# Kernel optimization log

Hardware: AMD Instinct MI355X
Metric: run time of the kernel (lower is better)

## Reference

```python
import jax, jax.numpy as jnp
import numpy as np

DIM = 1024
HEADS = 16
HEAD_DIM = DIM // HEADS
SCALE = HEAD_DIM ** -0.5


def setup_inputs() -> dict:
    key = jax.random.key(0)
    ks = jax.random.split(key, 6)
    B, N, C = 2, 2048, DIM
    q = jax.random.normal(ks[0], (B, N, C), dtype=jnp.float32)
    k = jax.random.normal(ks[1], (B, N, C), dtype=jnp.float32)
    v = jax.random.normal(ks[2], (B, N, C), dtype=jnp.float32)
    # torch nn.Linear weights: out = x @ W.T (+ b); qkv has no bias (qkv_bias=False)
    W_qkv = jax.random.normal(ks[3], (3 * C, 3 * C), dtype=jnp.float32) * (3 * C) ** -0.5
    W_proj = jax.random.normal(ks[4], (C, C), dtype=jnp.float32) * C ** -0.5
    b_proj = jax.random.normal(ks[5], (C,), dtype=jnp.float32) * 0.02
    return {"q": q, "k": k, "v": v, "W_qkv": W_qkv, "W_proj": W_proj, "b_proj": b_proj}


def reference(q, k, v, W_qkv, W_proj, b_proj):
    B, N, C = q.shape
    # fused QKV projection on concatenated [q,k,v] -> [B,N,3C]
    qkv = jnp.concatenate([q, k, v], axis=-1) @ W_qkv.T
    qkv = qkv.reshape(B, N, 3, HEADS, HEAD_DIM).transpose(2, 0, 3, 1, 4)  # [3,B,H,N,hd]
    qh, kh, vh = qkv[0], qkv[1], qkv[2]
    attn = jnp.einsum('bhqd,bhkd->bhqk', qh, kh) * SCALE
    attn = jax.nn.softmax(attn, axis=-1)  # attn_drop is identity (p=0)
    x = jnp.einsum('bhqk,bhkd->bhqd', attn, vh)  # [B,H,N,hd]
    x = x.transpose(0, 2, 1, 3).reshape(B, N, C)
    x = x @ W_proj.T + b_proj  # proj_drop is identity (p=0)
    return x
```

## Files before the change

kernel.cpp:

```cpp
#include <hip/hip_runtime.h>
#include <hip/hip_bf16.h>
#include <stdint.h>

#define HEADS 16
#define HD 64
#define SEQ 2048
#define BATCH 2
#define CDIM 1024
#define MROWS (BATCH*SEQ)
#define K3C (3*CDIM)
#define QSCALE 0.1803368801111244f

typedef __bf16 bf16x8 __attribute__((ext_vector_type(8)));
typedef float  f32x4  __attribute__((ext_vector_type(4)));

__device__ __forceinline__ unsigned short f2bf(float f) {
    __hip_bfloat16 h = __float2bfloat16(f);
    return __builtin_bit_cast(unsigned short, h);
}
__device__ __forceinline__ unsigned int pack2bf(float a, float b) {
    return (unsigned int)f2bf(a) | ((unsigned int)f2bf(b) << 16);
}
__device__ __forceinline__ bf16x8 frag(uint4 u) { return __builtin_bit_cast(bf16x8, u); }

__device__ __forceinline__ void async16(const unsigned short* g, unsigned short* lds) {
    __builtin_amdgcn_global_load_lds(
        (const __attribute__((address_space(1))) unsigned int*)g,
        (__attribute__((address_space(3))) unsigned int*)lds, 16, 0, 0);
}

__device__ __forceinline__ void dsr(uint4& d, unsigned addr, unsigned imm) {
    asm volatile("ds_read_b128 %0, %1 offset:%c2" : "=v"(d) : "v"(addr), "i"(imm));
}

__global__ void cast_all(const float* __restrict__ q, const float* __restrict__ k,
                         const float* __restrict__ v, const float* __restrict__ Wq,
                         const float* __restrict__ Wp,
                         unsigned short* __restrict__ A, unsigned short* __restrict__ Wqb,
                         unsigned short* __restrict__ Wpb)
{
    const int bid = blockIdx.x;
    const int t = threadIdx.x;
    if (bid < MROWS) {
        const float* srcs[3] = {q, k, v};
        #pragma unroll
        for (int i = 0; i < 3; ++i) {
            float4 f = *(const float4*)(srcs[i] + (size_t)bid*CDIM + t*4);
            ushort4 s;
            s.x = f2bf(f.x); s.y = f2bf(f.y); s.z = f2bf(f.z); s.w = f2bf(f.w);
            *(ushort4*)(A + (size_t)bid*K3C + i*CDIM + t*4) = s;
        }
    } else if (bid < MROWS + 9216) {
        int idx = (bid - MROWS)*256 + t;
        float4 f = ((const float4*)Wq)[idx];
        ushort4 s;
        s.x = f2bf(f.x); s.y = f2bf(f.y); s.z = f2bf(f.z); s.w = f2bf(f.w);
        ((ushort4*)Wqb)[idx] = s;
    } else {
        int idx = (bid - MROWS - 9216)*256 + t;
        float4 f = ((const float4*)Wp)[idx];
        ushort4 s;
        s.x = f2bf(f.x); s.y = f2bf(f.y); s.z = f2bf(f.z); s.w = f2bf(f.w);
        ((ushort4*)Wpb)[idx] = s;
    }
}

template<int EPI>
__global__ __launch_bounds__(256, 2)
void gemm_bt(const unsigned short* __restrict__ A, const unsigned short* __restrict__ B,
             int M, int N, int K,
             unsigned short* __restrict__ qh, unsigned short* __restrict__ kh,
             unsigned short* __restrict__ vt,
             const float* __restrict__ bias, float* __restrict__ out)
{
    __shared__ __attribute__((aligned(16))) unsigned short As[128*32];
    __shared__ __attribute__((aligned(16))) unsigned short Bs[128*32];
    const int tid  = threadIdx.x;
    const int wave = tid >> 6;
    const int lane = tid & 63;
    const int l15  = lane & 15;
    const int quad = lane >> 4;
    const int wm = (wave >> 1) * 64;
    const int wn = (wave & 1) * 64;
    const int m0 = blockIdx.x * 128;
    const int n0 = blockIdx.y * 128;

    f32x4 acc[4][4] = {};

    const int srow = tid >> 2;
    const int sc8  = (tid & 3) * 8;

    for (int k0 = 0; k0 < K; k0 += 32) {
        #pragma unroll
        for (int t = 0; t < 2; ++t) {
            int row = t*64 + srow;
            const unsigned short* ga = A + (size_t)(m0 + row)*K + k0 + sc8;
            const unsigned short* gb = B + (size_t)(n0 + row)*K + k0 + sc8;
            async16(ga, &As[(t*256 + wave*64)*8]);
            async16(gb, &Bs[(t*256 + wave*64)*8]);
        }
        __syncthreads();
        uint4 af[4], bfv[4];
        #pragma unroll
        for (int i = 0; i < 4; ++i) {
            af[i]  = *(const uint4*)&As[(wm + i*16 + l15)*32 + quad*8];
            bfv[i] = *(const uint4*)&Bs[(wn + i*16 + l15)*32 + quad*8];
        }
        #pragma unroll
        for (int mi = 0; mi < 4; ++mi)
            #pragma unroll
            for (int ni = 0; ni < 4; ++ni)
                acc[mi][ni] = __builtin_amdgcn_mfma_f32_16x16x32_bf16(
                    frag(af[mi]), frag(bfv[ni]), acc[mi][ni], 0, 0, 0);
        __syncthreads();
    }

    if constexpr (EPI == 0) {
        #pragma unroll
        for (int mi = 0; mi < 4; ++mi) {
            int row0 = m0 + wm + mi*16 + quad*4;
            int b  = row0 >> 11;
            int nq = row0 & 2047;
            #pragma unroll
            for (int ni = 0; ni < 4; ++ni) {
                int col   = n0 + wn + ni*16 + l15;
                int which = col >> 10;
                int h     = (col >> 6) & 15;
                int d     = col & 63;
                int bh    = b*HEADS + h;
                if (which == 2) {
                    ushort4 pv;
                    pv.x = f2bf(acc[mi][ni][0]);
                    pv.y = f2bf(acc[mi][ni][1]);
                    pv.z = f2bf(acc[mi][ni][2]);
                    pv.w = f2bf(acc[mi][ni][3]);
                    *(ushort4*)&vt[((size_t)bh*HD + d)*SEQ + nq] = pv;
                } else {
                    unsigned short* dst = (which == 0) ? qh : kh;
                    float sc = (which == 0) ? QSCALE : 1.0f;
                    #pragma unroll
                    for (int r = 0; r < 4; ++r)
                        dst[((size_t)bh*SEQ + nq + r)*HD + d] = f2bf(acc[mi][ni][r] * sc);
                }
            }
        }
    } else {
        #pragma unroll
        for (int mi = 0; mi < 4; ++mi) {
            int row0 = m0 + wm + mi*16 + quad*4;
            #pragma unroll
            for (int ni = 0; ni < 4; ++ni) {
                int col  = n0 + wn + ni*16 + l15;
                float bv = bias[col];
                #pragma unroll
                for (int r = 0; r < 4; ++r)
                    out[(size_t)(row0 + r)*N + col] = acc[mi][ni][r] + bv;
            }
        }
    }
}

#define NT48 48

__global__ __launch_bounds__(512, 2)
void gemm256_qkv(const unsigned short* __restrict__ A, const unsigned short* __restrict__ B,
                 unsigned short* __restrict__ qh, unsigned short* __restrict__ kh,
                 unsigned short* __restrict__ vt)
{
    __shared__ __attribute__((aligned(16))) unsigned short As[2*16384];
    __shared__ __attribute__((aligned(16))) unsigned short Bs[2*16384];

    const int tid  = threadIdx.x;
    const int wave = tid >> 6;
    const int lane = tid & 63;
    const int l15  = lane & 15;
    const int quad = lane >> 4;
    const int wr   = wave >> 2;
    const int wc   = wave & 3;

    const int id  = blockIdx.x;
    const int swz = (id & 7)*24 + (id >> 3);
    const int m0  = (swz & 15) * 256;
    const int n0  = (swz >> 4) * 256;

    int lrr[2], kel[2];
    #pragma unroll
    for (int j = 0; j < 2; ++j) {
        int p  = (j*512 + tid) * 16;
        int st = p >> 10;
        int q  = p & 1023;
        int ql = q ^ (((q >> 9) & 1) << 5);
        lrr[j] = (st >> 1)*16 + (ql >> 6);
        kel[j] = (st & 1)*32 + ((ql & 63) >> 1);
    }
    const int ldsc = wave*64*8;

    auto stageA = [&](int t, int g) {
        unsigned short* dst = As + (t & 1)*16384 + g*8192;
        #pragma unroll
        for (int j = 0; j < 2; ++j) {
            int grow = (lrr[j] >> 6)*128 + g*64 + (lrr[j] & 63);
            async16(A + (size_t)(m0 + grow)*K3C + t*64 + kel[j], dst + j*4096 + ldsc);
        }
    };
    auto stageB = [&](int t, int g) {
        unsigned short* dst = Bs + (t & 1)*16384 + g*8192;
        #pragma unroll
        for (int j = 0; j < 2; ++j) {
            int grow = (lrr[j] >> 5)*64 + g*32 + (lrr[j] & 31);
            async16(B + (size_t)(n0 + grow)*K3C + t*64 + kel[j], dst + j*4096 + ldsc);
        }
    };

    const unsigned lanebyte = (unsigned)((l15*64 + quad*16) ^ ((l15 & 8) << 2));
    const unsigned aAddr = (unsigned)(uintptr_t)&As[0] + lanebyte + (unsigned)(wr*8192);
    const unsigned bAddr = (unsigned)(uintptr_t)&Bs[0] + lanebyte + (unsigned)(wc*4096);

    f32x4 acc[8][4] = {};

    stageA(0, 0); stageB(0, 0); stageA(0, 1); stageB(0, 1);
    stageA(1, 0); stageB(1, 0); stageA(1, 1);
    asm volatile("s_waitcnt vmcnt(6)" ::: "memory");
    __builtin_amdgcn_s_barrier();

    for (int tt = 0; tt < NT48; tt += 2) {
        #pragma unroll
        for (int hb = 0; hb < 2; ++hb) {
            const int t = tt + hb;
            uint4 ar[4][2], bl[2][2], bh[2][2];

            #pragma unroll
            for (int mi = 0; mi < 4; ++mi)
                #pragma unroll
                for (int kc = 0; kc < 2; ++kc)
                    dsr(ar[mi][kc], aAddr, hb*32768 + (mi*2 + kc)*1024);
            #pragma unroll
            for (int ni = 0; ni < 2; ++ni)
                #pragma unroll
                for (int kc = 0; kc < 2; ++kc)
                    dsr(bl[ni][kc], bAddr, hb*32768 + (ni*2 + kc)*1024);
            if (t + 1 < NT48) stageB(t + 1, 1);
            __builtin_amdgcn_s_barrier();
            asm volatile("s_waitcnt lgkmcnt(0)" ::: "memory");
            __builtin_amdgcn_sched_barrier(0);
            __builtin_amdgcn_s_setprio(1);
            #pragma unroll
            for (int mi = 0; mi < 4; ++mi)
                #pragma unroll
                for (int ni = 0; ni < 2; ++ni)
                    #pragma unroll
                    for (int kc = 0; kc < 2; ++kc)
                        acc[mi][ni] = __builtin_amdgcn_mfma_f32_16x16x32_bf16(
                            frag(ar[mi][kc]), frag(bl[ni][kc]), acc[mi][ni], 0, 0, 0);
            __builtin_amdgcn_s_setprio(0);
            __builtin_amdgcn_s_barrier();

            #pragma unroll
            for (int ni = 0; ni < 2; ++ni)
                #pragma unroll
                for (int kc = 0; kc < 2; ++kc)
                    dsr(bh[ni][kc], bAddr, hb*32768 + 16384 + (ni*2 + kc)*1024);
            if (t + 2 < NT48) stageA(t + 2, 0);
            __builtin_amdgcn_s_barrier();
            asm volatile("s_waitcnt lgkmcnt(0)" ::: "memory");
            __builtin_amdgcn_sched_barrier(0);
            __builtin_amdgcn_s_setprio(1);
            #pragma unroll
            for (int mi = 0; mi < 4; ++mi)
                #pragma unroll
                for (int ni = 0; ni < 2; ++ni)
                    #pragma unroll
                    for (int kc = 0; kc < 2; ++kc)
                        acc[mi][ni+2] = __builtin_amdgcn_mfma_f32_16x16x32_bf16(
                            frag(ar[mi][kc]), frag(bh[ni][kc]), acc[mi][ni+2], 0, 0, 0);
            __builtin_amdgcn_s_setprio(0);
            __builtin_amdgcn_s_barrier();

            #pragma unroll
            for (int mi = 0; mi < 4; ++mi)
                #pragma unroll
                for (int kc = 0; kc < 2; ++kc)
                    dsr(ar[mi][kc], aAddr, hb*32768 + 16384 + (mi*2 + kc)*1024);
            if (t + 2 < NT48) stageB(t + 2, 0);
            __builtin_amdgcn_s_barrier();
            asm volatile("s_waitcnt lgkmcnt(0)" ::: "memory");
            __builtin_amdgcn_sched_barrier(0);
            __builtin_amdgcn_s_setprio(1);
            #pragma unroll
            for (int mi = 0; mi < 4; ++mi)
                #pragma unroll
                for (int ni = 0; ni < 2; ++ni)
                    #pragma unroll
                    for (int kc = 0; kc < 2; ++kc)
                        acc[mi+4][ni] = __builtin_amdgcn_mfma_f32_16x16x32_bf16(
                            frag(ar[mi][kc]), frag(bl[ni][kc]), acc[mi+4][ni], 0, 0, 0);
            __builtin_amdgcn_s_setprio(0);
            __builtin_amdgcn_s_barrier();

            if (t + 2 < NT48) stageA(t + 2, 1);
            if (t + 2 < NT48)      { asm volatile("s_waitcnt vmcnt(6)" ::: "memory"); }
            else if (t + 1 < NT48) { asm volatile("s_waitcnt vmcnt(0)" ::: "memory"); }
            __builtin_amdgcn_s_barrier();
            __builtin_amdgcn_s_setprio(1);
            #pragma unroll
            for (int mi = 0; mi < 4; ++mi)
                #pragma unroll
                for (int ni = 0; ni < 2; ++ni)
                    #pragma unroll
                    for (int kc = 0; kc < 2; ++kc)
                        acc[mi+4][ni+2] = __builtin_amdgcn_mfma_f32_16x16x32_bf16(
                            frag(ar[mi][kc]), frag(bh[ni][kc]), acc[mi+4][ni+2], 0, 0, 0);
            __builtin_amdgcn_s_setprio(0);
            __builtin_amdgcn_s_barrier();
        }
    }

    #pragma unroll
    for (int mi = 0; mi < 8; ++mi) {
        const int row0 = m0 + wr*128 + mi*16 + quad*4;
        const int b  = row0 >> 11;
        const int nq = row0 & 2047;
        #pragma unroll
        for (int ni = 0; ni < 4; ++ni) {
            const int col   = n0 + wc*64 + ni*16 + l15;
            const int which = col >> 10;
            const int h     = (col >> 6) & 15;
            const int d     = col & 63;
            const int bh_   = b*HEADS + h;
            if (which == 2) {
                ushort4 pv;
                pv.x = f2bf(acc[mi][ni][0]);
                pv.y = f2bf(acc[mi][ni][1]);
                pv.z = f2bf(acc[mi][ni][2]);
                pv.w = f2bf(acc[mi][ni][3]);
                *(ushort4*)&vt[((size_t)bh_*HD + d)*SEQ + nq] = pv;
            } else {
                unsigned short* dst = (which == 0) ? qh : kh;
                float sc = (which == 0) ? QSCALE : 1.0f;
                #pragma unroll
                for (int r = 0; r < 4; ++r)
                    dst[((size_t)bh_*SEQ + nq + r)*HD + d] = f2bf(acc[mi][ni][r] * sc);
            }
        }
    }
}

__global__ __launch_bounds__(256, 2)
void attention(const unsigned short* __restrict__ qh, const unsigned short* __restrict__ kh,
               const unsigned short* __restrict__ vt, unsigned short* __restrict__ xb)
{
    const int qt = blockIdx.x;
    const int h  = blockIdx.y;
    const int b  = blockIdx.z;
    const int bh = b*HEADS + h;
    const int tid  = threadIdx.x;
    const int wave = tid >> 6;
    const int lane = tid & 63;
    const int l15  = lane & 15;
    const int quad = lane >> 4;

    __shared__ __attribute__((aligned(16))) unsigned short Ks[2][64*64];
    __shared__ __attribute__((aligned(16))) unsigned short Vs[2][64*64];
    __shared__ __attribute__((aligned(16))) unsigned short Ps[4][2*16*72];

    const unsigned short* Qp = qh + ((size_t)bh*SEQ + qt*128 + wave*32)*HD;
    const unsigned short* Kp = kh + (size_t)bh*SEQ*HD;
    const unsigned short* Vp = vt + (size_t)bh*HD*SEQ;

    auto stage = [&](int kt, int bufI) {
        #pragma unroll
        for (int t = 0; t < 2; ++t) {
            int c  = t*256 + wave*64 + lane;
            int r  = c >> 3;
            int cc = (c & 7) ^ (r & 7);
            async16(Kp + (size_t)(kt*64 + r)*HD + cc*8,
                    &Ks[bufI][(t*256 + wave*64)*8]);
            async16(Vp + (size_t)r*SEQ + kt*64 + cc*8,
                    &Vs[bufI][(t*256 + wave*64)*8]);
        }
    };

    stage(0, 0);

    uint4 qf[2][2];
    #pragma unroll
    for (int g = 0; g < 2; ++g) {
        qf[g][0] = *(const uint4*)(Qp + (size_t)(g*16 + l15)*HD + quad*8);
        qf[g][1] = *(const uint4*)(Qp + (size_t)(g*16 + l15)*HD + 32 + quad*8);
    }

    f32x4 o[2][4] = {};
    float m_s[2] = {-INFINITY, -INFINITY};
    float l_s[2] = {0.f, 0.f};

    unsigned short* Pw = Ps[wave];
    const int x7 = l15 & 7;

    for (int kt = 0; kt < SEQ/64; ++kt) {
        stage((kt + 1) & 31, (kt + 1) & 1);
        asm volatile("s_waitcnt vmcnt(4)" ::: "memory");
        asm volatile("s_barrier" ::: "memory");

        const unsigned short* Kb = Ks[kt & 1];
        const unsigned short* Vb = Vs[kt & 1];

        f32x4 s[2][4];
        #pragma unroll
        for (int st = 0; st < 4; ++st) {
            int rb = st*16 + l15;
            uint4 kf0 = *(const uint4*)&Kb[(rb*8 + (quad ^ x7))*8];
            uint4 kf1 = *(const uint4*)&Kb[(rb*8 + ((4 + quad) ^ x7))*8];
            #pragma unroll
            for (int g = 0; g < 2; ++g) {
                f32x4 z = {};
                z = __builtin_amdgcn_mfma_f32_16x16x32_bf16(frag(kf0), frag(qf[g][0]), z, 0, 0, 0);
                z = __builtin_amdgcn_mfma_f32_16x16x32_bf16(frag(kf1), frag(qf[g][1]), z, 0, 0, 0);
                s[g][st] = z;
            }
        }

        #pragma unroll
        for (int g = 0; g < 2; ++g) {
            float mloc = s[g][0][0];
            #pragma unroll
            for (int st = 0; st < 4; ++st)
                #pragma unroll
                for (int r = 0; r < 4; ++r)
                    mloc = fmaxf(mloc, s[g][st][r]);
            mloc = fmaxf(mloc, __shfl_xor(mloc, 16));
            mloc = fmaxf(mloc, __shfl_xor(mloc, 32));

            float mn = fmaxf(m_s[g], mloc);
            float al = __builtin_amdgcn_exp2f(m_s[g] - mn);
            m_s[g] = mn;

            float rs = 0.f;
            float p[4][4];
            #pragma unroll
            for (int st = 0; st < 4; ++st)
                #pragma unroll
                for (int r = 0; r < 4; ++r) {
                    p[st][r] = __builtin_amdgcn_exp2f(s[g][st][r] - mn);
                    rs += p[st][r];
                }
            rs += __shfl_xor(rs, 16);
            rs += __shfl_xor(rs, 32);
            l_s[g] = al*l_s[g] + rs;

            #pragma unroll
            for (int st = 0; st < 4; ++st)
                #pragma unroll
                for (int r = 0; r < 4; ++r)
                    o[g][st][r] *= al;

            #pragma unroll
            for (int st = 0; st < 4; ++st) {
                uint2 pk;
                pk.x = pack2bf(p[st][0], p[st][1]);
                pk.y = pack2bf(p[st][2], p[st][3]);
                *(uint2*)&Pw[g*1152 + l15*72 + st*16 + quad*4] = pk;
            }
        }
        asm volatile("s_waitcnt lgkmcnt(0)" ::: "memory");

        uint4 pB[2][2];
        #pragma unroll
        for (int g = 0; g < 2; ++g) {
            pB[g][0] = *(const uint4*)&Pw[g*1152 + l15*72 + quad*8];
            pB[g][1] = *(const uint4*)&Pw[g*1152 + l15*72 + 32 + quad*8];
        }

        #pragma unroll
        for (int st = 0; st < 4; ++st) {
            int rb = st*16 + l15;
            uint4 vf0 = *(const uint4*)&Vb[(rb*8 + (quad ^ x7))*8];
            uint4 vf1 = *(const uint4*)&Vb[(rb*8 + ((4 + quad) ^ x7))*8];
            #pragma unroll
            for (int g = 0; g < 2; ++g) {
                o[g][st] = __builtin_amdgcn_mfma_f32_16x16x32_bf16(frag(vf0), frag(pB[g][0]), o[g][st], 0, 0, 0);
                o[g][st] = __builtin_amdgcn_mfma_f32_16x16x32_bf16(frag(vf1), frag(pB[g][1]), o[g][st], 0, 0, 0);
            }
        }

        asm volatile("s_barrier" ::: "memory");
    }

    #pragma unroll
    for (int g = 0; g < 2; ++g) {
        float inv = 1.0f / l_s[g];
        #pragma unroll
        for (int st = 0; st < 4; ++st) {
            uint2 pk;
            pk.x = pack2bf(o[g][st][0]*inv, o[g][st][1]*inv);
            pk.y = pack2bf(o[g][st][2]*inv, o[g][st][3]*inv);
            *(uint2*)&Pw[g*1152 + l15*72 + st*16 + quad*4] = pk;
        }
    }
    asm volatile("s_waitcnt lgkmcnt(0)" ::: "memory");

    const int qr = lane >> 2;
    const int dd = (lane & 3) * 16;
    #pragma unroll
    for (int g = 0; g < 2; ++g) {
        uint4 oa = *(const uint4*)&Pw[g*1152 + qr*72 + dd];
        uint4 ob = *(const uint4*)&Pw[g*1152 + qr*72 + dd + 8];
        const int mrow = b*SEQ + qt*128 + wave*32 + g*16 + qr;
        *(uint4*)&xb[(size_t)mrow*CDIM + h*HD + dd]     = oa;
        *(uint4*)&xb[(size_t)mrow*CDIM + h*HD + dd + 8] = ob;
    }
}

extern "C" void kernel_launch(void* const* d_in, const int* in_sizes, int n_in,
                              void* d_out, int out_size, void* d_ws, size_t ws_size,
                              hipStream_t stream)
{
    const float* q  = (const float*)d_in[0];
    const float* k  = (const float*)d_in[1];
    const float* v  = (const float*)d_in[2];
    const float* Wq = (const float*)d_in[3];
    const float* Wp = (const float*)d_in[4];
    const float* bp = (const float*)d_in[5];
    float* out = (float*)d_out;

    char* p = (char*)d_ws;
    auto carve = [&](size_t bytes) { char* r = p; p += (bytes + 255) & ~(size_t)255; return r; };
    unsigned short* Abuf   = (unsigned short*)carve((size_t)MROWS*K3C*2);
    unsigned short* Wqkvb  = (unsigned short*)carve((size_t)K3C*K3C*2);
    unsigned short* Wprojb = (unsigned short*)carve((size_t)CDIM*CDIM*2);
    unsigned short* qhb    = (unsigned short*)carve((size_t)BATCH*HEADS*SEQ*HD*2);
    unsigned short* khb    = (unsigned short*)carve((size_t)BATCH*HEADS*SEQ*HD*2);
    unsigned short* vtb    = (unsigned short*)carve((size_t)BATCH*HEADS*SEQ*HD*2);
    unsigned short* xbuf   = (unsigned short*)carve((size_t)MROWS*CDIM*2);

    cast_all<<<MROWS + 9216 + 1024, 256, 0, stream>>>(q, k, v, Wq, Wp, Abuf, Wqkvb, Wprojb);

    gemm256_qkv<<<dim3(192), 512, 0, stream>>>(Abuf, Wqkvb, qhb, khb, vtb);

    attention<<<dim3(SEQ/128, HEADS, BATCH), 256, 0, stream>>>(qhb, khb, vtb, xbuf);

    gemm_bt<1><<<dim3(MROWS/128, CDIM/128), 256, 0, stream>>>(
        xbuf, Wprojb, MROWS, CDIM, CDIM, nullptr, nullptr, nullptr, bp, out);
}
```

Before: 300.5 us.

## Retile QKV GEMM to 256x192 tiles for 256 blocks matching CU count

The QKV projection GEMM moves from 256x256 tiles (192 blocks) to 256x192 tiles (256 blocks), so the grid matches the 256 CUs of MI355X and fewer CUs sit idle. Staging is simplified to a single per-k-step stage function issuing 7 async loads, placed before the last MFMA phase instead of spread across phases. MFMA loops are reordered so kc is outermost. The smaller N tile lowers arithmetic intensity and reduces how much global-load latency each block can hide.

```diff
diff --git a/kernel.cpp b/kernel.cpp
--- a/kernel.cpp
+++ b/kernel.cpp
@@ -168,7 +168,7 @@
                  unsigned short* __restrict__ vt)
 {
     __shared__ __attribute__((aligned(16))) unsigned short As[2*16384];
-    __shared__ __attribute__((aligned(16))) unsigned short Bs[2*16384];
+    __shared__ __attribute__((aligned(16))) unsigned short Bs[2*12288];
 
     const int tid  = threadIdx.x;
     const int wave = tid >> 6;
@@ -179,137 +179,129 @@
     const int wc   = wave & 3;
 
     const int id  = blockIdx.x;
-    const int swz = (id & 7)*24 + (id >> 3);
+    const int swz = (id & 7)*32 + (id >> 3);
     const int m0  = (swz & 15) * 256;
-    const int n0  = (swz >> 4) * 256;
-
-    int lrr[2], kel[2];
+    const int n0  = (swz >> 4) * 192;
+
+    size_t aSrc[4]; size_t bSrc[3];
     #pragma unroll
-    for (int j = 0; j < 2; ++j) {
-        int p  = (j*512 + tid) * 16;
-        int st = p >> 10;
-        int q  = p & 1023;
+    for (int u = 0; u < 4; ++u) {
+        int P  = u*8192 + tid*16;
+        int st = P >> 10, q = P & 1023;
         int ql = q ^ (((q >> 9) & 1) << 5);
-        lrr[j] = (st >> 1)*16 + (ql >> 6);
-        kel[j] = (st & 1)*32 + ((ql & 63) >> 1);
-    }
-    const int ldsc = wave*64*8;
-
-    auto stageA = [&](int t, int g) {
-        unsigned short* dst = As + (t & 1)*16384 + g*8192;
-        #pragma unroll
-        for (int j = 0; j < 2; ++j) {
-            int grow = (lrr[j] >> 6)*128 + g*64 + (lrr[j] & 63);
-            async16(A + (size_t)(m0 + grow)*K3C + t*64 + kel[j], dst + j*4096 + ldsc);
-        }
+        int row = m0 + (st >> 1)*16 + (ql >> 6);
+        int kel = (st & 1)*32 + ((ql & 63) >> 1);
+        aSrc[u] = (size_t)row*K3C + kel;
+    }
+    #pragma unroll
+    for (int u = 0; u < 3; ++u) {
+        int P  = u*8192 + tid*16;
+        int st = P >> 10, q = P & 1023;
+        int ql = q ^ (((q >> 9) & 1) << 5);
+        int row = n0 + (st >> 1)*16 + (ql >> 6);
+        int kel = (st & 1)*32 + ((ql & 63) >> 1);
+        bSrc[u] = (size_t)row*K3C + kel;
+    }
+    const int wdst = wave*512;
+
+    auto stage = [&](int t) {
+        const int hb = t & 1;
+        #pragma unroll
+        for (int u = 0; u < 4; ++u)
+            async16(A + aSrc[u] + t*64, As + hb*16384 + u*4096 + wdst);
+        #pragma unroll
+        for (int u = 0; u < 3; ++u)
+            async16(B + bSrc[u] + t*64, Bs + hb*12288 + u*4096 + wdst);
     };
-    auto stageB = [&](int t, int g) {
-        unsigned short* dst = Bs + (t & 1)*16384 + g*8192;
-        #pragma unroll
-        for (int j = 0; j < 2; ++j) {
-            int grow = (lrr[j] >> 5)*64 + g*32 + (lrr[j] & 31);
-            async16(B + (size_t)(n0 + grow)*K3C + t*64 + kel[j], dst + j*4096 + ldsc);
-        }
-    };
 
     const unsigned lanebyte = (unsigned)((l15*64 + quad*16) ^ ((l15 & 8) << 2));
-    const unsigned aAddr = (unsigned)(uintptr_t)&As[0] + lanebyte + (unsigned)(wr*8192);
-    const unsigned bAddr = (unsigned)(uintptr_t)&Bs[0] + lanebyte + (unsigned)(wc*4096);
-
-    f32x4 acc[8][4] = {};
-
-    stageA(0, 0); stageB(0, 0); stageA(0, 1); stageB(0, 1);
-    stageA(1, 0); stageB(1, 0); stageA(1, 1);
-    asm volatile("s_waitcnt vmcnt(6)" ::: "memory");
+    const unsigned aAddr = (unsigned)(uintptr_t)&As[0] + lanebyte + (unsigned)(wr*16384);
+    const unsigned bAddr = (unsigned)(uintptr_t)&Bs[0] + lanebyte + (unsigned)(wc*6144);
+
+    f32x4 acc[8][3] = {};
+
+    stage(0); stage(1);
+    asm volatile("s_waitcnt vmcnt(7)" ::: "memory");
     __builtin_amdgcn_s_barrier();
 
     for (int tt = 0; tt < NT48; tt += 2) {
         #pragma unroll
         for (int hb = 0; hb < 2; ++hb) {
             const int t = tt + hb;
-            uint4 ar[4][2], bl[2][2], bh[2][2];
+            uint4 ar[4][2], bl[2][2], bh[2];
 
             #pragma unroll
             for (int mi = 0; mi < 4; ++mi)
                 #pragma unroll
                 for (int kc = 0; kc < 2; ++kc)
-                    dsr(ar[mi][kc], aAddr, hb*32768 + (mi*2 + kc)*1024);
+                    dsr(ar[mi][kc], aAddr, hb*32768 + mi*2048 + kc*1024);
             #pragma unroll
             for (int ni = 0; ni < 2; ++ni)
                 #pragma unroll
                 for (int kc = 0; kc < 2; ++kc)
-                    dsr(bl[ni][kc], bAddr, hb*32768 + (ni*2 + kc)*1024);
-            if (t + 1 < NT48) stageB(t + 1, 1);
+                    dsr(bl[ni][kc], bAddr, hb*24576 + ni*2048 + kc*1024);
             __builtin_amdgcn_s_barrier();
             asm volatile("s_waitcnt lgkmcnt(0)" ::: "memory");
             __builtin_amdgcn_sched_barrier(0);
             __builtin_amdgcn_s_setprio(1);
             #pragma unroll
-            for (int mi = 0; mi < 4; ++mi)
-                #pragma unroll
-                for (int ni = 0; ni < 2; ++ni)
+            for (int kc = 0; kc < 2; ++kc)
+                #pragma unroll
+                for (int mi = 0; mi < 4; ++mi)
                     #pragma unroll
-                    for (int kc = 0; kc < 2; ++kc)
+                    for (int ni = 0; ni < 2; ++ni)
                         acc[mi][ni] = __builtin_amdgcn_mfma_f32_16x16x32_bf16(
                             frag(ar[mi][kc]), frag(bl[ni][kc]), acc[mi][ni], 0, 0, 0);
             __builtin_amdgcn_s_setprio(0);
             __builtin_amdgcn_s_barrier();
 
             #pragma unroll
-            for (int ni = 0; ni < 2; ++ni)
-                #pragma unroll
-                for (int kc = 0; kc < 2; ++kc)
-                    dsr(bh[ni][kc], bAddr, hb*32768 + 16384 + (ni*2 + kc)*1024);
-            if (t + 2 < NT48) stageA(t + 2, 0);
+            for (int kc = 0; kc < 2; ++kc)
+                dsr(bh[kc], bAddr, hb*24576 + 2*2048 + kc*1024);
             __builtin_amdgcn_s_barrier();
             asm volatile("s_waitcnt lgkmcnt(0)" ::: "memory");
             __builtin_amdgcn_sched_barrier(0);
             __builtin_amdgcn_s_setprio(1);
             #pragma unroll
+            for (int kc = 0; kc < 2; ++kc)
+                #pragma unroll
+                for (int mi = 0; mi < 4; ++mi)
+                    acc[mi][2] = __builtin_amdgcn_mfma_f32_16x16x32_bf16(
+                        frag(ar[mi][kc]), frag(bh[kc]), acc[mi][2], 0, 0, 0);
+            __builtin_amdgcn_s_setprio(0);
+            __builtin_amdgcn_s_barrier();
+
+            #pragma unroll
             for (int mi = 0; mi < 4; ++mi)
                 #pragma unroll
-                for (int ni = 0; ni < 2; ++ni)
-                    #pragma unroll
-                    for (int kc = 0; kc < 2; ++kc)
-                        acc[mi][ni+2] = __builtin_amdgcn_mfma_f32_16x16x32_bf16(
-                            frag(ar[mi][kc]), frag(bh[ni][kc]), acc[mi][ni+2], 0, 0, 0);
-            __builtin_amdgcn_s_setprio(0);
-            __builtin_amdgcn_s_barrier();
-
-            #pragma unroll
-            for (int mi = 0; mi < 4; ++mi)
-                #pragma unroll
                 for (int kc = 0; kc < 2; ++kc)
-                    dsr(ar[mi][kc], aAddr, hb*32768 + 16384 + (mi*2 + kc)*1024);
-            if (t + 2 < NT48) stageB(t + 2, 0);
+                    dsr(ar[mi][kc], aAddr, hb*32768 + (4 + mi)*2048 + kc*1024);
             __builtin_amdgcn_s_barrier();
             asm volatile("s_waitcnt lgkmcnt(0)" ::: "memory");
             __builtin_amdgcn_sched_barrier(0);
             __builtin_amdgcn_s_setprio(1);
             #pragma unroll
-            for (int mi = 0; mi < 4; ++mi)
-                #pragma unroll
-                for (int ni = 0; ni < 2; ++ni)
+            for (int kc = 0; kc < 2; ++kc)
+                #pragma unroll
+                for (int mi = 0; mi < 4; ++mi)
                     #pragma unroll
-                    for (int kc = 0; kc < 2; ++kc)
+                    for (int ni = 0; ni < 2; ++ni)
                         acc[mi+4][ni] = __builtin_amdgcn_mfma_f32_16x16x32_bf16(
                             frag(ar[mi][kc]), frag(bl[ni][kc]), acc[mi+4][ni], 0, 0, 0);
             __builtin_amdgcn_s_setprio(0);
             __builtin_amdgcn_s_barrier();
 
-            if (t + 2 < NT48) stageA(t + 2, 1);
-            if (t + 2 < NT48)      { asm volatile("s_waitcnt vmcnt(6)" ::: "memory"); }
+            if (t + 2 < NT48)      { stage(t + 2);
+                                     asm volatile("s_waitcnt vmcnt(7)" ::: "memory"); }
             else if (t + 1 < NT48) { asm volatile("s_waitcnt vmcnt(0)" ::: "memory"); }
             __builtin_amdgcn_s_barrier();
             __builtin_amdgcn_s_setprio(1);
             #pragma unroll
-            for (int mi = 0; mi < 4; ++mi)
-                #pragma unroll
-                for (int ni = 0; ni < 2; ++ni)
-                    #pragma unroll
-                    for (int kc = 0; kc < 2; ++kc)
-                        acc[mi+4][ni+2] = __builtin_amdgcn_mfma_f32_16x16x32_bf16(
-                            frag(ar[mi][kc]), frag(bh[ni][kc]), acc[mi+4][ni+2], 0, 0, 0);
+            for (int kc = 0; kc < 2; ++kc)
+                #pragma unroll
+                for (int mi = 0; mi < 4; ++mi)
+                    acc[mi+4][2] = __builtin_amdgcn_mfma_f32_16x16x32_bf16(
+                        frag(ar[mi][kc]), frag(bh[kc]), acc[mi+4][2], 0, 0, 0);
             __builtin_amdgcn_s_setprio(0);
             __builtin_amdgcn_s_barrier();
         }
@@ -321,8 +313,8 @@
         const int b  = row0 >> 11;
         const int nq = row0 & 2047;
         #pragma unroll
-        for (int ni = 0; ni < 4; ++ni) {
-            const int col   = n0 + wc*64 + ni*16 + l15;
+        for (int ni = 0; ni < 3; ++ni) {
+            const int col   = n0 + wc*48 + ni*16 + l15;
             const int which = col >> 10;
             const int h     = (col >> 6) & 15;
             const int d     = col & 63;
@@ -534,7 +526,7 @@
 
     cast_all<<<MROWS + 9216 + 1024, 256, 0, stream>>>(q, k, v, Wq, Wp, Abuf, Wqkvb, Wprojb);
 
-    gemm256_qkv<<<dim3(192), 512, 0, stream>>>(Abuf, Wqkvb, qhb, khb, vtb);
+    gemm256_qkv<<<dim3(256), 512, 0, stream>>>(Abuf, Wqkvb, qhb, khb, vtb);
 
     attention<<<dim3(SEQ/128, HEADS, BATCH), 256, 0, stream>>>(qhb, khb, vtb, xbuf);
 
```

Result: no change. 300.4 us (-0.1%).
